# Kernel optimization log

Hardware: AMD Instinct MI355X
Metric: run time of the kernel (lower is better)

## Reference

```python
import jax, jax.numpy as jnp
import numpy as np

B, NPTS, NBASIS, DIM, H, CH = 8, 1024, 8, 8, 512, 16
EPSILON = 1000.0
P = 2
VOLUME = 2.0 ** DIM  # MC domain [-1,1]^dim


def setup_inputs() -> dict:
    key = jax.random.key(0)
    ks = jax.random.split(key, 10)
    s = jax.random.uniform(ks[0], (NPTS, DIM), dtype=jnp.float32) * 2.0 - 1.0  # MC samples in [-1,1]^dim
    x = jax.random.uniform(ks[1], (1, DIM), dtype=jnp.float32) * 2.0 - 1.0     # eval point
    Wfirst = jax.random.normal(ks[2], (DIM, H), dtype=jnp.float32) / np.sqrt(DIM)
    bfirst = jax.random.normal(ks[3], (H,), dtype=jnp.float32) * 0.01
    Wb = jax.random.normal(ks[4], (NBASIS, H, H), dtype=jnp.float32) / np.sqrt(H)
    bb = jax.random.normal(ks[5], (NBASIS, H), dtype=jnp.float32) * 0.01
    Wlast = jax.random.normal(ks[6], (H, CH), dtype=jnp.float32) / np.sqrt(H)
    blast = jax.random.normal(ks[7], (CH,), dtype=jnp.float32) * 0.01
    Wf = jax.random.normal(ks[8], (DIM, CH), dtype=jnp.float32) / np.sqrt(DIM)
    bf = jax.random.normal(ks[9], (CH,), dtype=jnp.float32) * 0.01
    return dict(s=s, x=x, Wfirst=Wfirst, bfirst=bfirst, Wb=Wb, bb=bb,
                Wlast=Wlast, blast=blast, Wf=Wf, bf=bf)


def _basis_all(pts, Wfirst, bfirst, Wb, bb, Wlast, blast):
    # pts: [M, DIM] -> all n basis nets, batch-repeated: [NBASIS, B, M, CH]
    a0 = jax.nn.elu(jnp.einsum('md,dh->mh', pts, Wfirst) + bfirst)          # [M, H]
    a0 = jnp.broadcast_to(a0[None], (B,) + a0.shape)                         # [B, M, H] (repeat over batch)
    a1 = jax.nn.elu(jnp.einsum('bmh,ihk->ibmk', a0, Wb) + bb[:, None, None, :])  # [n, B, M, H]
    return jnp.einsum('ibmk,kc->ibmc', a1, Wlast) + blast                    # [n, B, M, CH]


def reference(s, x, Wfirst, bfirst, Wb, bb, Wlast, blast, Wf, bf):
    # func(s): linear map realizing the projected function  [NPTS, CH]
    f_s = jnp.einsum('nd,dc->nc', s, Wf) + bf
    basis_s = _basis_all(s, Wfirst, bfirst, Wb, bb, Wlast, blast)            # [n, B, NPTS, CH]
    diff = f_s[None, None] - basis_s                                          # broadcast over n, B
    # Monte Carlo integral of (func - basis_i)^p over [-1,1]^dim, per channel
    integral = VOLUME * jnp.mean(diff ** P, axis=-2)                          # [n, B, CH]
    norm_pc = integral ** (1.0 / P)                                           # Lp norm per channel
    norm_b = jnp.sum(jnp.abs(norm_pc) ** P, axis=-1, keepdims=True) ** (1.0 / P)  # [n, B, 1]
    mu = jnp.where(norm_b <= EPSILON, norm_b, 0.0)                            # [n, B, 1]
    basis_x = _basis_all(x, Wfirst, bfirst, Wb, bb, Wlast, blast)[:, :, 0, :]  # [n, B, CH]
    out = jnp.sum(mu * basis_x, axis=0)                                       # [B, CH]
    normalization = 1e-7 + jnp.sum(mu, axis=0)                                # [B, 1]
    return out / normalization
```

## Files before the change

kernel.cpp:

```cpp
#include <hip/hip_runtime.h>

typedef _Float16 half8 __attribute__((ext_vector_type(8)));
typedef float f32x4 __attribute__((ext_vector_type(4)));
typedef float f32x16 __attribute__((ext_vector_type(16)));
typedef unsigned int u32x4 __attribute__((ext_vector_type(4)));

#define NPTS 1024
#define NB 8
#define HDIM 512
#define CH 16
#define RT 1056

#define OFF_WBF 0u
#define OFF_A0F (4u*1024u*1024u)
#define A0SZ    (64u*RT*16u)
#define OFF_WLF (OFF_A0F + A0SZ)
#define OFF_FS  (OFF_WLF + 16384u)
#define OFF_PP  (OFF_FS + 65536u)
#define PPSZ    (8u*4u*RT*16u*4u)
#define OFF_IS  (OFF_PP + PPSZ)
#define OFF_BX  (OFF_IS + 64u)

__device__ __forceinline__ float elu(float z) { return z > 0.f ? z : expm1f(z); }

__global__ __launch_bounds__(256) void kPrep(const float* __restrict__ s,
    const float* __restrict__ x, const float* __restrict__ Wfirst,
    const float* __restrict__ bfirst, const float* __restrict__ Wb,
    const float* __restrict__ Wlast, const float* __restrict__ Wf,
    const float* __restrict__ bf,
    _Float16* __restrict__ Wbf, _Float16* __restrict__ Wlf,
    _Float16* __restrict__ a0f, float* __restrict__ f_s,
    float* __restrict__ Isum) {
  __shared__ __align__(16) float sm[8192];
  int b = blockIdx.x, t = threadIdx.x;
  if (b < 1024) {
    int i = b >> 7, koct = (b >> 1) & 63, n = (b & 1) * 256 + t;
    const float* src = Wb + ((size_t)i * 512 + koct * 8) * 512 + n;
    float v[8];
#pragma unroll
    for (int j = 0; j < 8; ++j) v[j] = src[j * 512];
    union { _Float16 h[8]; u32x4 u; } hu;
#pragma unroll
    for (int j = 0; j < 8; ++j) hu.h[j] = (_Float16)v[j];
    *(u32x4*)(Wbf + ((size_t)(i * 64 + koct) * 512 + n) * 8) = hu.u;
  } else if (b < 1288) {
    int rr = t >> 6, tl = t & 63;
    int m = (b - 1024) * 4 + rr;
    float* sv = &sm[rr * 8];
    if (tl < 8) sv[tl] = (m < 1024) ? s[m * 8 + tl] : (m == 1024 ? x[tl] : 0.f);
    __syncthreads();
    size_t o = ((size_t)tl * RT + m) * 8;
    if (m <= 1024) {
      float acc[8];
#pragma unroll
      for (int jj = 0; jj < 8; ++jj) acc[jj] = bfirst[8 * tl + jj];
#pragma unroll
      for (int d = 0; d < 8; ++d) {
        float sd = sv[d];
        f32x4 w0 = *(const f32x4*)&Wfirst[d * 512 + 8 * tl];
        f32x4 w1 = *(const f32x4*)&Wfirst[d * 512 + 8 * tl + 4];
#pragma unroll
        for (int e = 0; e < 4; ++e) { acc[e] += sd * w0[e]; acc[4 + e] += sd * w1[e]; }
      }
      union { _Float16 h[8]; u32x4 u; } hu;
#pragma unroll
      for (int jj = 0; jj < 8; ++jj) hu.h[jj] = (_Float16)elu(acc[jj]);
      *(u32x4*)(a0f + o) = hu.u;
      if (m < 1024 && tl < 16) {
        float a = bf[tl];
#pragma unroll
        for (int d = 0; d < 8; ++d) a += sv[d] * Wf[d * 16 + tl];
        f_s[m * 16 + tl] = a;
      }
    } else {
      u32x4 z;
#pragma unroll
      for (int e = 0; e < 4; ++e) z[e] = 0u;
      *(u32x4*)(a0f + o) = z;
    }
  } else {
    if (t < 8) Isum[t] = 0.f;
#pragma unroll
    for (int it = 0; it < 32; ++it) sm[t + 256 * it] = Wlast[t + 256 * it];
    __syncthreads();
#pragma unroll
    for (int p = 0; p < 4; ++p) {
      int oi = p * 256 + t;
      int ko = oi >> 4, ch = oi & 15;
      union { _Float16 h[8]; u32x4 u; } hu;
#pragma unroll
      for (int jj = 0; jj < 8; ++jj) hu.h[jj] = (_Float16)sm[(ko * 8 + jj) * 16 + ch];
      *(u32x4*)(Wlf + oi * 8) = hu.u;
    }
  }
}

__global__ __launch_bounds__(256, 4) void kB(const _Float16* __restrict__ Wbf,
    const _Float16* __restrict__ a0f, const _Float16* __restrict__ Wlf,
    const float* __restrict__ bb, float* __restrict__ Pp) {
  __shared__ u32x4 SC[512];
  __shared__ float S2[32][16];
  int t = threadIdx.x, b = blockIdx.x;
  int i = b & 7, r = b >> 3;
  int nq = r & 3, mt = r >> 2;
  int m0 = mt * 32;
  int w = t >> 6, lane = t & 63, ln = lane & 31, q = lane >> 5, q4 = lane >> 4;
  int nw = nq * 128 + w * 32;

  const u32x4* a4 = (const u32x4*)a0f;
  const u32x4* b4 = (const u32x4*)Wbf;
  int ma = m0 + ln, nb = nw + ln, ib = i * 64;

  f32x16 acc;
#pragma unroll
  for (int rr = 0; rr < 16; ++rr) acc[rr] = 0.f;

  u32x4 pa[4][2], pb[4][2];
#pragma unroll
  for (int st = 0; st < 3; ++st) {
    int k0 = st * 4 + q, k1 = k0 + 2;
    pa[st][0] = a4[k0 * RT + ma];
    pa[st][1] = a4[k1 * RT + ma];
    pb[st][0] = b4[(size_t)(ib + k0) * 512 + nb];
    pb[st][1] = b4[(size_t)(ib + k1) * 512 + nb];
  }
#pragma unroll
  for (int ks = 0; ks < 16; ++ks) {
    int sl = ks & 3;
    acc = __builtin_amdgcn_mfma_f32_32x32x16_f16(
        __builtin_bit_cast(half8, pa[sl][0]), __builtin_bit_cast(half8, pb[sl][0]), acc, 0, 0, 0);
    acc = __builtin_amdgcn_mfma_f32_32x32x16_f16(
        __builtin_bit_cast(half8, pa[sl][1]), __builtin_bit_cast(half8, pb[sl][1]), acc, 0, 0, 0);
    if (ks < 13) {
      int sn = (ks + 3) & 3;
      int k0 = (ks + 3) * 4 + q, k1 = k0 + 2;
      pa[sn][0] = a4[k0 * RT + ma];
      pa[sn][1] = a4[k1 * RT + ma];
      pb[sn][0] = b4[(size_t)(ib + k0) * 512 + nb];
      pb[sn][1] = b4[(size_t)(ib + k1) * 512 + nb];
    }
  }

  ((float*)S2)[t] = 0.f;
  ((float*)S2)[t + 256] = 0.f;
  float bcol = bb[i * 512 + nw + ln];
  _Float16* scr = (_Float16*)&SC[w * 128];
#pragma unroll
  for (int rr = 0; rr < 16; ++rr) {
    int row = (rr & 3) + 8 * (rr >> 2) + 4 * q;
    float a1 = elu(acc[rr] + bcol);
    int oi = (row >> 4) * 64 + (ln >> 3) * 16 + (row & 15);
    scr[oi * 8 + (ln & 7)] = (_Float16)a1;
  }
  __syncthreads();

  const u32x4* s4 = &SC[w * 128];
  const u32x4* w4 = (const u32x4*)Wlf;
  int ch = lane & 15;
  half8 wv = __builtin_bit_cast(half8, w4[(size_t)((nw >> 3) + q4) * 16 + ch]);
#pragma unroll
  for (int mt2 = 0; mt2 < 2; ++mt2) {
    f32x4 D2;
#pragma unroll
    for (int rr = 0; rr < 4; ++rr) D2[rr] = 0.f;
    half8 pv = __builtin_bit_cast(half8, s4[mt2 * 64 + q4 * 16 + ch]);
    D2 = __builtin_amdgcn_mfma_f32_16x16x32_f16(pv, wv, D2, 0, 0, 0);
#pragma unroll
    for (int rr = 0; rr < 4; ++rr)
      atomicAdd(&S2[mt2 * 16 + q4 * 4 + rr][ch], D2[rr]);
  }
  __syncthreads();
  for (int o = t; o < 512; o += 256) {
    int m = o >> 4, c2 = o & 15;
    Pp[((size_t)(i * 4 + nq) * RT + m0 + m) * 16 + c2] = S2[m][c2];
  }
}

__global__ __launch_bounds__(256) void kRed(const float* __restrict__ Pp,
    const float* __restrict__ f_s, const float* __restrict__ blast,
    float* __restrict__ Isum, float* __restrict__ basisx) {
  __shared__ float wsum[4];
  int b = blockIdx.x, t = threadIdx.x;
  int i = b / 33, mt = b - i * 33;
  const float* P0 = Pp + (size_t)(i * 4) * RT * 16;
  const size_t PS = (size_t)RT * 16;
  if (mt == 32) {
    if (t < 16) {
      size_t o = (size_t)1024 * 16 + t;
      basisx[i * 16 + t] = P0[o] + P0[PS + o] + P0[2 * PS + o] + P0[3 * PS + o] + blast[t];
    }
    return;
  }
  float loc = 0.f;
#pragma unroll
  for (int p = 0; p < 2; ++p) {
    int item = t + p * 256;
    int m = mt * 32 + (item >> 4), ch = item & 15;
    size_t o = (size_t)m * 16 + ch;
    float bs = P0[o] + P0[PS + o] + P0[2 * PS + o] + P0[3 * PS + o] + blast[ch];
    float d = f_s[o] - bs;
    loc += d * d;
  }
  loc += __shfl_xor(loc, 1, 64);
  loc += __shfl_xor(loc, 2, 64);
  loc += __shfl_xor(loc, 4, 64);
  loc += __shfl_xor(loc, 8, 64);
  loc += __shfl_xor(loc, 16, 64);
  loc += __shfl_xor(loc, 32, 64);
  int lane = t & 63, w = t >> 6;
  if (lane == 0) wsum[w] = loc;
  __syncthreads();
  if (t == 0) atomicAdd(&Isum[i], wsum[0] + wsum[1] + wsum[2] + wsum[3]);
}

__global__ __launch_bounds__(128) void kFin(const float* __restrict__ Isum,
    const float* __restrict__ basisx, float* __restrict__ out) {
  __shared__ float muL[8];
  int t = threadIdx.x;
  if (t < 8) {
    float nb = 0.5f * sqrtf(Isum[t]);
    muL[t] = (nb <= 1000.0f) ? nb : 0.f;
  }
  __syncthreads();
  int ch = t & 15;
  float num = 0.f, den = 1e-7f;
#pragma unroll
  for (int i = 0; i < NB; ++i) {
    num += muL[i] * basisx[i * 16 + ch];
    den += muL[i];
  }
  out[t] = num / den;
}

extern "C" void kernel_launch(void* const* d_in, const int* in_sizes, int n_in,
                              void* d_out, int out_size, void* d_ws, size_t ws_size,
                              hipStream_t stream) {
  const float* s      = (const float*)d_in[0];
  const float* x      = (const float*)d_in[1];
  const float* Wfirst = (const float*)d_in[2];
  const float* bfirst = (const float*)d_in[3];
  const float* Wb     = (const float*)d_in[4];
  const float* bb     = (const float*)d_in[5];
  const float* Wlast  = (const float*)d_in[6];
  const float* blast  = (const float*)d_in[7];
  const float* Wf     = (const float*)d_in[8];
  const float* bf     = (const float*)d_in[9];

  char* ws = (char*)d_ws;
  _Float16* Wbf = (_Float16*)(ws + OFF_WBF);
  _Float16* a0f = (_Float16*)(ws + OFF_A0F);
  _Float16* Wlf = (_Float16*)(ws + OFF_WLF);
  float* f_s    = (float*)(ws + OFF_FS);
  float* Pp     = (float*)(ws + OFF_PP);
  float* Isum   = (float*)(ws + OFF_IS);
  float* basisx = (float*)(ws + OFF_BX);
  float* out    = (float*)d_out;

  kPrep<<<1289, 256, 0, stream>>>(s, x, Wfirst, bfirst, Wb, Wlast, Wf, bf,
                                  Wbf, Wlf, a0f, f_s, Isum);
  kB<<<1056, 256, 0, stream>>>(Wbf, a0f, Wlf, bb, Pp);
  kRed<<<264, 256, 0, stream>>>(Pp, f_s, blast, Isum, basisx);
  kFin<<<1, 128, 0, stream>>>(Isum, basisx, out);
}
```

Baseline: 115.4 us.

## Stage GEMM tiles through LDS with async global_load_lds double buffering

The main basis GEMM kernel now loads A and B tiles into shared memory with direct global-to-LDS loads, double-buffered across eight K stages, rather than each wave loading its own operands into registers. Each block covers a 64x128 output tile, with each wave computing two 32x32 accumulators. This halves the block count and gives A and B operands reuse across waves. The row padding grows to 1088 to fit the 64-row tiles, so the prep kernel launches a few more blocks. The larger LDS footprint and the occupancy hint lowered from 4 to 3 reduce how many blocks can be resident at once.

Result: faster. 110.0 us (-4.7%).

```diff
diff --git a/kernel.cpp b/kernel.cpp
--- a/kernel.cpp
+++ b/kernel.cpp
@@ -9,7 +9,7 @@
 #define NB 8
 #define HDIM 512
 #define CH 16
-#define RT 1056
+#define RT 1088
 
 #define OFF_WBF 0u
 #define OFF_A0F (4u*1024u*1024u)
@@ -17,11 +17,17 @@
 #define OFF_WLF (OFF_A0F + A0SZ)
 #define OFF_FS  (OFF_WLF + 16384u)
 #define OFF_PP  (OFF_FS + 65536u)
-#define PPSZ    (8u*4u*RT*16u*4u)
+#define PPSZ    (32u*RT*16u*4u)
 #define OFF_IS  (OFF_PP + PPSZ)
 #define OFF_BX  (OFF_IS + 64u)
 
 __device__ __forceinline__ float elu(float z) { return z > 0.f ? z : expm1f(z); }
+
+__device__ __forceinline__ void gl16(const void* g, void* l) {
+  __builtin_amdgcn_global_load_lds(
+      (const __attribute__((address_space(1))) unsigned int*)g,
+      (__attribute__((address_space(3))) unsigned int*)l, 16, 0, 0);
+}
 
 __global__ __launch_bounds__(256) void kPrep(const float* __restrict__ s,
     const float* __restrict__ x, const float* __restrict__ Wfirst,
@@ -43,7 +49,7 @@
 #pragma unroll
     for (int j = 0; j < 8; ++j) hu.h[j] = (_Float16)v[j];
     *(u32x4*)(Wbf + ((size_t)(i * 64 + koct) * 512 + n) * 8) = hu.u;
-  } else if (b < 1288) {
+  } else if (b < 1296) {
     int rr = t >> 6, tl = t & 63;
     int m = (b - 1024) * 4 + rr;
     float* sv = &sm[rr * 8];
@@ -95,84 +101,103 @@
   }
 }
 
-__global__ __launch_bounds__(256, 4) void kB(const _Float16* __restrict__ Wbf,
+
+#define STAGE(buf, ks) do {                                                          \
+    int kb_ = (ks) * 8;                                                              \
+    char* lA_ = lds + (buf) * 8192;                                                  \
+    char* lB_ = lds + 16384 + (buf) * 16384;                                         \
+    gl16(&a4[(size_t)(kb_ + (t >> 6)) * RT + m0 + (t & 63)], lA_ + t * 16);          \
+    gl16(&a4[(size_t)(kb_ + 4 + (t >> 6)) * RT + m0 + (t & 63)], lA_ + 4096 + t * 16); \
+    gl16(&b4[(size_t)(ib + kb_ + (t >> 7)) * 512 + n0 + (t & 127)], lB_ + t * 16);   \
+    gl16(&b4[(size_t)(ib + kb_ + 2 + (t >> 7)) * 512 + n0 + (t & 127)], lB_ + 4096 + t * 16); \
+    gl16(&b4[(size_t)(ib + kb_ + 4 + (t >> 7)) * 512 + n0 + (t & 127)], lB_ + 8192 + t * 16); \
+    gl16(&b4[(size_t)(ib + kb_ + 6 + (t >> 7)) * 512 + n0 + (t & 127)], lB_ + 12288 + t * 16); \
+  } while (0)
+
+#define COMP(buf) do {                                                               \
+    const u32x4* Ab_ = (const u32x4*)(lds + (buf) * 8192);                           \
+    const u32x4* Bb_ = (const u32x4*)(lds + 16384 + (buf) * 16384);                  \
+    _Pragma("unroll")                                                                \
+    for (int kk = 0; kk < 4; ++kk) {                                                 \
+      int ko_ = 2 * kk + q;                                                          \
+      u32x4 av = Ab_[ko_ * 64 + wr * 32 + ln];                                       \
+      u32x4 bv0 = Bb_[ko_ * 128 + nc + ln];                                          \
+      u32x4 bv1 = Bb_[ko_ * 128 + nc + 32 + ln];                                     \
+      acc0 = __builtin_amdgcn_mfma_f32_32x32x16_f16(                                 \
+          __builtin_bit_cast(half8, av), __builtin_bit_cast(half8, bv0), acc0, 0, 0, 0); \
+      acc1 = __builtin_amdgcn_mfma_f32_32x32x16_f16(                                 \
+          __builtin_bit_cast(half8, av), __builtin_bit_cast(half8, bv1), acc1, 0, 0, 0); \
+    }                                                                                \
+  } while (0)
+
+__global__ __launch_bounds__(256, 3) void kB(const _Float16* __restrict__ Wbf,
     const _Float16* __restrict__ a0f, const _Float16* __restrict__ Wlf,
     const float* __restrict__ bb, float* __restrict__ Pp) {
-  __shared__ u32x4 SC[512];
-  __shared__ float S2[32][16];
+  __shared__ __align__(16) char lds[49152];
   int t = threadIdx.x, b = blockIdx.x;
   int i = b & 7, r = b >> 3;
   int nq = r & 3, mt = r >> 2;
-  int m0 = mt * 32;
-  int w = t >> 6, lane = t & 63, ln = lane & 31, q = lane >> 5, q4 = lane >> 4;
-  int nw = nq * 128 + w * 32;
-
+  int m0 = mt * 64, n0 = nq * 128;
+  int w = t >> 6, lane = t & 63, ln = lane & 31, q = lane >> 5;
+  int wr = w & 1, nc = (w >> 1) * 64;
+  int ib = i * 64;
   const u32x4* a4 = (const u32x4*)a0f;
   const u32x4* b4 = (const u32x4*)Wbf;
-  int ma = m0 + ln, nb = nw + ln, ib = i * 64;
-
-  f32x16 acc;
-#pragma unroll
-  for (int rr = 0; rr < 16; ++rr) acc[rr] = 0.f;
-
-  u32x4 pa[4][2], pb[4][2];
-#pragma unroll
-  for (int st = 0; st < 3; ++st) {
-    int k0 = st * 4 + q, k1 = k0 + 2;
-    pa[st][0] = a4[k0 * RT + ma];
-    pa[st][1] = a4[k1 * RT + ma];
-    pb[st][0] = b4[(size_t)(ib + k0) * 512 + nb];
-    pb[st][1] = b4[(size_t)(ib + k1) * 512 + nb];
-  }
-#pragma unroll
-  for (int ks = 0; ks < 16; ++ks) {
-    int sl = ks & 3;
-    acc = __builtin_amdgcn_mfma_f32_32x32x16_f16(
-        __builtin_bit_cast(half8, pa[sl][0]), __builtin_bit_cast(half8, pb[sl][0]), acc, 0, 0, 0);
-    acc = __builtin_amdgcn_mfma_f32_32x32x16_f16(
-        __builtin_bit_cast(half8, pa[sl][1]), __builtin_bit_cast(half8, pb[sl][1]), acc, 0, 0, 0);
-    if (ks < 13) {
-      int sn = (ks + 3) & 3;
-      int k0 = (ks + 3) * 4 + q, k1 = k0 + 2;
-      pa[sn][0] = a4[k0 * RT + ma];
-      pa[sn][1] = a4[k1 * RT + ma];
-      pb[sn][0] = b4[(size_t)(ib + k0) * 512 + nb];
-      pb[sn][1] = b4[(size_t)(ib + k1) * 512 + nb];
-    }
-  }
-
-  ((float*)S2)[t] = 0.f;
-  ((float*)S2)[t + 256] = 0.f;
-  float bcol = bb[i * 512 + nw + ln];
-  _Float16* scr = (_Float16*)&SC[w * 128];
+
+  f32x16 acc0, acc1;
+#pragma unroll
+  for (int rr = 0; rr < 16; ++rr) { acc0[rr] = 0.f; acc1[rr] = 0.f; }
+
+  STAGE(0, 0);
+  __syncthreads();
+#pragma unroll
+  for (int s = 0; s < 8; ++s) {
+    if (s < 7) STAGE((s + 1) & 1, s + 1);
+    COMP(s & 1);
+    __syncthreads();
+  }
+
+  float* S2f = (float*)(lds + 16384);
+#pragma unroll
+  for (int z = 0; z < 4; ++z) S2f[t + 256 * z] = 0.f;
+
+  _Float16* scr = (_Float16*)(lds + w * 4096);
+  float bcA = bb[(size_t)i * 512 + n0 + nc + ln];
+  float bcB = bb[(size_t)i * 512 + n0 + nc + 32 + ln];
 #pragma unroll
   for (int rr = 0; rr < 16; ++rr) {
     int row = (rr & 3) + 8 * (rr >> 2) + 4 * q;
-    float a1 = elu(acc[rr] + bcol);
-    int oi = (row >> 4) * 64 + (ln >> 3) * 16 + (row & 15);
-    scr[oi * 8 + (ln & 7)] = (_Float16)a1;
-  }
-  __syncthreads();
-
-  const u32x4* s4 = &SC[w * 128];
+    float aA = elu(acc0[rr] + bcA);
+    float aB = elu(acc1[rr] + bcB);
+    int mt2 = row >> 4, m16 = row & 15;
+    scr[(mt2 * 128 + (ln >> 3) * 16 + m16) * 8 + (ln & 7)] = (_Float16)aA;
+    scr[(mt2 * 128 + (4 + (ln >> 3)) * 16 + m16) * 8 + (ln & 7)] = (_Float16)aB;
+  }
+  __syncthreads();
+
+  const u32x4* s4 = (const u32x4*)(lds + w * 4096);
   const u32x4* w4 = (const u32x4*)Wlf;
-  int ch = lane & 15;
-  half8 wv = __builtin_bit_cast(half8, w4[(size_t)((nw >> 3) + q4) * 16 + ch]);
+  int ch = lane & 15, q4 = lane >> 4;
+  int hb = (n0 + nc) >> 3;
+  half8 wv0 = __builtin_bit_cast(half8, w4[(size_t)(hb + q4) * 16 + ch]);
+  half8 wv1 = __builtin_bit_cast(half8, w4[(size_t)(hb + 4 + q4) * 16 + ch]);
 #pragma unroll
   for (int mt2 = 0; mt2 < 2; ++mt2) {
-    f32x4 D2;
-#pragma unroll
-    for (int rr = 0; rr < 4; ++rr) D2[rr] = 0.f;
-    half8 pv = __builtin_bit_cast(half8, s4[mt2 * 64 + q4 * 16 + ch]);
-    D2 = __builtin_amdgcn_mfma_f32_16x16x32_f16(pv, wv, D2, 0, 0, 0);
+    f32x4 D;
+#pragma unroll
+    for (int rr = 0; rr < 4; ++rr) D[rr] = 0.f;
+    half8 p0 = __builtin_bit_cast(half8, s4[mt2 * 128 + q4 * 16 + ch]);
+    half8 p1 = __builtin_bit_cast(half8, s4[mt2 * 128 + (4 + q4) * 16 + ch]);
+    D = __builtin_amdgcn_mfma_f32_16x16x32_f16(p0, wv0, D, 0, 0, 0);
+    D = __builtin_amdgcn_mfma_f32_16x16x32_f16(p1, wv1, D, 0, 0, 0);
 #pragma unroll
     for (int rr = 0; rr < 4; ++rr)
-      atomicAdd(&S2[mt2 * 16 + q4 * 4 + rr][ch], D2[rr]);
-  }
-  __syncthreads();
-  for (int o = t; o < 512; o += 256) {
+      atomicAdd(&S2f[(wr * 32 + mt2 * 16 + q4 * 4 + rr) * 16 + ch], D[rr]);
+  }
+  __syncthreads();
+  for (int o = t; o < 1024; o += 256) {
     int m = o >> 4, c2 = o & 15;
-    Pp[((size_t)(i * 4 + nq) * RT + m0 + m) * 16 + c2] = S2[m][c2];
+    Pp[((size_t)(i * 4 + nq) * RT + m0 + m) * 16 + c2] = S2f[m * 16 + c2];
   }
 }
 
@@ -256,9 +281,9 @@
   float* basisx = (float*)(ws + OFF_BX);
   float* out    = (float*)d_out;
 
-  kPrep<<<1289, 256, 0, stream>>>(s, x, Wfirst, bfirst, Wb, Wlast, Wf, bf,
+  kPrep<<<1297, 256, 0, stream>>>(s, x, Wfirst, bfirst, Wb, Wlast, Wf, bf,
                                   Wbf, Wlf, a0f, f_s, Isum);
-  kB<<<1056, 256, 0, stream>>>(Wbf, a0f, Wlf, bb, Pp);
+  kB<<<544, 256, 0, stream>>>(Wbf, a0f, Wlf, bb, Pp);
   kRed<<<264, 256, 0, stream>>>(Pp, f_s, blast, Isum, basisx);
   kFin<<<1, 128, 0, stream>>>(Isum, basisx, out);
 }
```
